# Kernel optimization log

Hardware: AMD Instinct MI355X
Metric: run time of the kernel (lower is better)

## Reference

```python
import jax, jax.numpy as jnp
import numpy as np

B, L, H, T, C = 4, 256, 768, 16, 6
SIM_THR = 0.0
EPS_LN = 1e-5


def layer_norm(x, g, b):
    m = x.mean(-1, keepdims=True)
    v = ((x - m) ** 2).mean(-1, keepdims=True)
    return (x - m) / jnp.sqrt(v + EPS_LN) * g + b


def setup_inputs() -> dict:
    key = jax.random.key(0)
    ks = jax.random.split(key, 20)
    s = 0.02
    embeddings = jax.random.normal(ks[0], (B, L, H), jnp.float32)
    masks = jnp.ones((B, L, L), jnp.float32)
    asp_st = jax.random.randint(ks[1], (B, T), 0, 12)
    asp_ed = asp_st + jax.random.randint(ks[2], (B, T), 0, 3)
    opi_st = jax.random.randint(ks[3], (B, T), 0, 12)
    opi_ed = opi_st + jax.random.randint(ks[4], (B, T), 0, 3)
    sent_id = jax.random.randint(ks[5], (B, T), 2, 5)
    return {
        "embeddings": embeddings, "masks": masks,
        "asp_st": asp_st, "asp_ed": asp_ed, "opi_st": opi_st, "opi_ed": opi_ed,
        "sent_id": sent_id,
        "edge_embed": jax.random.normal(ks[6], (2, H), jnp.float32) * s,
        "W_tp": jax.random.normal(ks[7], (2 * H + 3, H), jnp.float32) * s,
        "b_tp": jnp.zeros((H,), jnp.float32),
        "W_attn": jax.random.normal(ks[8], (3 * H, 1), jnp.float32) * s,
        "b_attn": jnp.zeros((1,), jnp.float32),
        "W_gat": jax.random.normal(ks[9], (2 * H, H), jnp.float32) * s,
        "b_gat": jnp.zeros((H,), jnp.float32),
        "gamma0": jnp.ones((H,), jnp.float32), "beta0": jnp.zeros((H,), jnp.float32),
        "W1": jax.random.normal(ks[10], (2 * H, L), jnp.float32) * s,
        "bl1": jnp.zeros((L,), jnp.float32),
        "gamma1": jnp.ones((L,), jnp.float32), "beta1": jnp.zeros((L,), jnp.float32),
        "Wc": jax.random.normal(ks[11], (L, C), jnp.float32) * s,
        "bc": jnp.zeros((C,), jnp.float32),
        "Wc1": jax.random.normal(ks[12], (L, 2), jnp.float32) * s,
        "bc1": jnp.zeros((2,), jnp.float32),
    }


def _triplet_enhance(emb_b, a_st, a_ed, o_st, o_ed, sid,
                     edge_embed, W_tp, b_tp, W_attn, b_attn, W_gat, b_gat):
    # emb_b: [L,H]; span ints: [T]
    pos = jnp.arange(L)
    am = (pos[None, :] >= a_st[:, None]) & (pos[None, :] <= a_ed[:, None])  # [T,L]
    om = (pos[None, :] >= o_st[:, None]) & (pos[None, :] <= o_ed[:, None])
    amf = am.astype(emb_b.dtype)
    omf = om.astype(emb_b.dtype)
    asp = (amf @ emb_b) / amf.sum(1, keepdims=True)  # [T,H] span-mean
    opi = (omf @ emb_b) / omf.sum(1, keepdims=True)
    sv = jax.nn.one_hot(sid - 2, 3, dtype=emb_b.dtype)  # [T,3]
    nf = jnp.concatenate([asp, opi, sv], -1) @ W_tp + b_tp  # [T,H]

    # cosine similarity between triplet nodes
    nrm = nf / jnp.maximum(jnp.linalg.norm(nf, axis=-1, keepdims=True), 1e-8)
    sim = nrm @ nrm.T
    eye = jnp.eye(T, dtype=bool)
    ok = (sim > SIM_THR) & ~eye
    m0 = ok & (a_st[:, None] == a_st[None, :]) & (a_ed[:, None] == a_ed[None, :])
    m1 = ok & (o_st[:, None] == o_st[None, :]) & (o_ed[:, None] == o_ed[None, :])
    # edge (i,j): src=i, tgt=j -> incoming mask indexed [tgt, src, etype]
    emask = jnp.stack([m0.T, m1.T], axis=-1)  # [T,T,2]

    E = edge_embed  # [2,H]
    cc = jnp.concatenate([
        jnp.broadcast_to(nf[:, None, None, :], (T, T, 2, H)),   # target feats
        jnp.broadcast_to(nf[None, :, None, :], (T, T, 2, H)),   # source feats
        jnp.broadcast_to(E[None, None, :, :], (T, T, 2, H)),
    ], -1)  # [T,T,2,3H]
    scores = (jax.nn.leaky_relu(cc, 0.2) @ W_attn)[..., 0] + b_attn[0]  # [T,T,2]
    neg = jnp.where(emask, scores, -1e9)
    attn = jax.nn.softmax(neg.reshape(T, -1), axis=-1).reshape(T, T, 2)
    msg = jnp.concatenate([
        jnp.broadcast_to(nf[:, None, :], (T, 2, H)),
        jnp.broadcast_to(E[None, :, :], (T, 2, H)),
    ], -1)  # [src, etype, 2H]
    agg = jnp.einsum('tse,sef->tf', attn, msg)
    upd = jax.nn.relu(agg @ W_gat + b_gat)
    has_in = emask.any(axis=(1, 2))
    new_nf = jnp.where(has_in[:, None], upd, nf)
    has_edges = emask.any().astype(emb_b.dtype)  # original skips scatter if no edges
    center = (a_st + o_st) // 2
    return emb_b.at[center].add(new_nf * has_edges)


def reference(embeddings, masks, asp_st, asp_ed, opi_st, opi_ed, sent_id,
              edge_embed, W_tp, b_tp, W_attn, b_attn, W_gat, b_gat,
              gamma0, beta0, W1, bl1, gamma1, beta1, Wc, bc, Wc1, bc1):
    emb1 = layer_norm(embeddings, gamma0, beta0)
    emb = jax.vmap(_triplet_enhance,
                   in_axes=(0, 0, 0, 0, 0, 0) + (None,) * 7)(
        emb1, asp_st, asp_ed, opi_st, opi_ed, sent_id,
        edge_embed, W_tp, b_tp, W_attn, b_attn, W_gat, b_gat)

    # cat([feat_exp, feat_expT]) @ W1  ==  emb@W1[:H] (rows) + emb@W1[H:] (cols)
    A = jnp.einsum('bih,hk->bik', emb, W1[:H])
    Bm = jnp.einsum('bjh,hk->bjk', emb, W1[H:])
    hidden = A[:, :, None, :] + Bm[:, None, :, :] + bl1  # [B,L,L,L]
    hidden = jax.nn.gelu(layer_norm(hidden, gamma1, beta1), approximate=False)
    logits = (hidden @ Wc + bc) * masks[..., None]    # [B,L,L,C]
    logits1 = (hidden @ Wc1 + bc1) * masks[..., None]  # [B,L,L,2]
    return jnp.concatenate([logits, logits1], -1)
```

## Files before the change

### kernel.cpp

```cpp
#include <hip/hip_runtime.h>

__device__ __forceinline__ unsigned short f2bf(float f) {
    union { float f; unsigned u; } v; v.f = f;
    unsigned u = v.u;
    unsigned r = (u + 0x7fffu + ((u >> 16) & 1u)) >> 16;
    return (unsigned short)r;
}
__device__ __forceinline__ float bfup(int x) {
    union { unsigned u; float f; } v; v.u = ((unsigned)(unsigned short)x) << 16; return v.f;
}

typedef __attribute__((ext_vector_type(8))) short short8;
typedef __attribute__((ext_vector_type(4))) float floatx4;

#define Bn 4
#define Ln 256
#define Hn 768
#define Tn 16
#define PITCH 288
#define PN 784

__global__ __launch_bounds__(256) void k_pre(const float* __restrict__ x,
                                             const float* __restrict__ g,
                                             const float* __restrict__ be,
                                             float* __restrict__ out,
                                             const float* __restrict__ W1,
                                             unsigned short* __restrict__ w1t,
                                             const float* __restrict__ Wc,
                                             const float* __restrict__ Wc1,
                                             const float* __restrict__ g1,
                                             const float* __restrict__ b1,
                                             unsigned short* __restrict__ wfg,
                                             const int* __restrict__ ast_, const int* __restrict__ aed_,
                                             const int* __restrict__ ost_, const int* __restrict__ oed_,
                                             const int* __restrict__ sid_,
                                             float* __restrict__ xv,
                                             float* __restrict__ nf,
                                             float* __restrict__ hedge) {
    int bid = blockIdx.x, tid = threadIdx.x;
    if (bid < 1024) {
        int row = bid;
        const float* xr = x + (size_t)row * Hn;
        float v0 = xr[tid], v1 = xr[tid + 256], v2 = xr[tid + 512];
        float s = v0 + v1 + v2;
        float q = v0 * v0 + v1 * v1 + v2 * v2;
        __shared__ float sm[4], qm[4];
        for (int o = 32; o > 0; o >>= 1) { s += __shfl_down(s, o); q += __shfl_down(q, o); }
        if ((tid & 63) == 0) { sm[tid >> 6] = s; qm[tid >> 6] = q; }
        __syncthreads();
        float S = sm[0] + sm[1] + sm[2] + sm[3];
        float Q = qm[0] + qm[1] + qm[2] + qm[3];
        float mean = S * (1.f / 768.f);
        float rstd = rsqrtf(Q * (1.f / 768.f) - mean * mean + 1e-5f);
        float* o0 = out + (size_t)row * Hn;
        o0[tid]       = (v0 - mean) * rstd * g[tid]       + be[tid];
        o0[tid + 256] = (v1 - mean) * rstd * g[tid + 256] + be[tid + 256];
        o0[tid + 512] = (v2 - mean) * rstd * g[tid + 512] + be[tid + 512];
    } else if (bid < 1408) {
        __shared__ float tile[32][33];
        int idx = bid - 1024;
        int kt = idx % 24, nt = idx / 24;
        int k0 = kt * 32, n0 = nt * 32;
        int rowoff = (n0 < 256) ? 0 : 768;
        int col0 = n0 & 255;
        int r = tid >> 3, c = (tid & 7) * 4;
        float4 v = *(const float4*)(W1 + (size_t)(rowoff + k0 + r) * 256 + col0 + c);
        tile[r][c] = v.x; tile[r][c + 1] = v.y; tile[r][c + 2] = v.z; tile[r][c + 3] = v.w;
        __syncthreads();
        ushort4 o;
        o.x = f2bf(tile[c][r]); o.y = f2bf(tile[c + 1][r]);
        o.z = f2bf(tile[c + 2][r]); o.w = f2bf(tile[c + 3][r]);
        *(ushort4*)(w1t + (size_t)(n0 + r) * 768 + k0 + c) = o;
    } else if (bid == 1408) {
#pragma unroll
        for (int u = 0; u < 2; ++u) {
            int e = tid + u * 256;
            int s = e >> 6, l = e & 63;
            int qq2 = l >> 4, nn2 = l & 15;
            short8 wv;
#pragma unroll
            for (int t = 0; t < 8; ++t) {
                int k = s * 32 + qq2 * 8 + t;
                float v = (nn2 < 6) ? Wc[k * 6 + nn2] : ((nn2 < 8) ? Wc1[k * 2 + (nn2 - 6)] : 0.f);
                wv[t] = (short)f2bf(v);
            }
            *(short8*)(wfg + e * 8) = wv;
        }
        wfg[4096 + tid] = f2bf(g1[tid]);
        wfg[4352 + tid] = f2bf(b1[tid]);
        if (tid < 4) hedge[tid] = 0.f;
    } else {
        __shared__ float rstdA[3], rstdO[3], cc[2];
        __shared__ float sred[4], qred[4];
        int n = bid - 1409, b = n >> 4;
        int ast = ast_[n], aed = aed_[n], ost = ost_[n], oed = oed_[n], sid = sid_[n];
        int na = aed - ast + 1, no2 = oed - ost + 1;
        if (tid == 0) { cc[0] = 0.f; cc[1] = 0.f; }
        __syncthreads();
        for (int slot = 0; slot < 6; ++slot) {
            int isA = slot < 3;
            int off = isA ? slot : slot - 3;
            int cnt = isA ? na : no2;
            int row = (isA ? ast : ost) + off;
            if (off < cnt) {
                const float* xr = x + (size_t)(b * 256 + row) * Hn;
                float v0 = xr[tid], v1 = xr[tid + 256], v2 = xr[tid + 512];
                float s = v0 + v1 + v2;
                float q = v0 * v0 + v1 * v1 + v2 * v2;
                for (int o = 32; o > 0; o >>= 1) { s += __shfl_down(s, o); q += __shfl_down(q, o); }
                if ((tid & 63) == 0) { sred[tid >> 6] = s; qred[tid >> 6] = q; }
            }
            __syncthreads();
            if (off < cnt && tid == 0) {
                float S = sred[0] + sred[1] + sred[2] + sred[3];
                float Q = qred[0] + qred[1] + qred[2] + qred[3];
                float mean = S * (1.f / 768.f);
                float rstd = rsqrtf(Q * (1.f / 768.f) - mean * mean + 1e-5f);
                if (isA) { rstdA[off] = rstd; cc[0] += mean * rstd; }
                else     { rstdO[off] = rstd; cc[1] += mean * rstd; }
            }
            __syncthreads();
        }
        float ai = 1.f / (float)na, oi = 1.f / (float)no2;
        float cA = cc[0] * ai, cO = cc[1] * oi;
        float* xrr = xv + (size_t)n * 1568;
        const float* eb = x + (size_t)b * Ln * Hn;
        for (int r = tid; r < 1568; r += 256) {
            float v;
            if (r < 768) {
                float sa = 0.f;
                for (int l = 0; l < na; ++l) sa = fmaf(eb[(ast + l) * Hn + r], rstdA[l], sa);
                v = fmaf(g[r], sa * ai - cA, be[r]);
            } else if (r < 1536) {
                int h = r - 768;
                float so = 0.f;
                for (int l = 0; l < no2; ++l) so = fmaf(eb[(ost + l) * Hn + h], rstdO[l], so);
                v = fmaf(g[h], so * oi - cO, be[h]);
            } else if (r < 1539) {
                v = (sid - 2 == r - 1536) ? 1.f : 0.f;
            } else {
                v = 0.f;
            }
            xrr[r] = v;
        }
        float* nr = nf + (size_t)n * Hn;
        nr[tid] = 0.f; nr[tid + 256] = 0.f; nr[tid + 512] = 0.f;
    }
}

__global__ __launch_bounds__(256) void k_skinny(const float* __restrict__ A,
                                                const float* __restrict__ B,
                                                const float* __restrict__ bias,
                                                float* __restrict__ C,
                                                int Kpad, int Kb, int Kc) {
    __shared__ float At[32][33], Bt[32][33];
    int tid = threadIdx.x;
    int n0 = blockIdx.x * 32, m0 = blockIdx.y * 32, z = blockIdx.z;
    int kbeg = z * Kc;
    int kend = kbeg + Kc; if (kend > Kpad) kend = Kpad;
    int lr = tid >> 3, lc = (tid & 7) * 4;
    int tm = tid >> 3, tn4 = (tid & 7) * 4;
    float acc0 = 0.f, acc1 = 0.f, acc2 = 0.f, acc3 = 0.f;
    for (int k0 = kbeg; k0 < kend; k0 += 32) {
        float4 av = *(const float4*)(A + (size_t)(m0 + lr) * Kpad + k0 + lc);
        At[lr][lc] = av.x; At[lr][lc + 1] = av.y; At[lr][lc + 2] = av.z; At[lr][lc + 3] = av.w;
        int gk = k0 + lr;
        float4 bv = {0.f, 0.f, 0.f, 0.f};
        if (gk < Kb) bv = *(const float4*)(B + (size_t)gk * 768 + n0 + lc);
        Bt[lr][lc] = bv.x; Bt[lr][lc + 1] = bv.y; Bt[lr][lc + 2] = bv.z; Bt[lr][lc + 3] = bv.w;
        __syncthreads();
#pragma unroll
        for (int k = 0; k < 32; ++k) {
            float a = At[tm][k];
            acc0 = fmaf(a, Bt[k][tn4], acc0);
            acc1 = fmaf(a, Bt[k][tn4 + 1], acc1);
            acc2 = fmaf(a, Bt[k][tn4 + 2], acc2);
            acc3 = fmaf(a, Bt[k][tn4 + 3], acc3);
        }
        __syncthreads();
    }
    if (z == 0) {
        acc0 += bias[n0 + tn4];
        acc1 += bias[n0 + tn4 + 1];
        acc2 += bias[n0 + tn4 + 2];
        acc3 += bias[n0 + tn4 + 3];
    }
    float* dst = C + (size_t)(m0 + tm) * 768 + n0 + tn4;
    atomicAdd(&dst[0], acc0);
    atomicAdd(&dst[1], acc1);
    atomicAdd(&dst[2], acc2);
    atomicAdd(&dst[3], acc3);
}

__global__ __launch_bounds__(256) void k_graph(const float* __restrict__ nf,
                                               const int* __restrict__ ast_, const int* __restrict__ aed_,
                                               const int* __restrict__ ost_, const int* __restrict__ oed_,
                                               const float* __restrict__ E,
                                               const float* __restrict__ Wat,
                                               const float* __restrict__ bat,
                                               int* __restrict__ hasin, float* __restrict__ hasedge,
                                               float* __restrict__ agg, float* __restrict__ raw) {
    int n = blockIdx.x, b = n >> 4, t = n & 15, tid = threadIdx.x;
    __shared__ float nfs[16][PN];
    __shared__ float dotS[16], n2S[16], qS[16];
    __shared__ float pT_s, rr0_s, rr1_s;
    __shared__ int asts[16], aeds[16], osts[16], oeds[16];
    __shared__ float wss[16];
    __shared__ float aes0, aes1;
    const float* nfb = nf + (size_t)b * 16 * Hn;
    if (tid < 16) {
        int m = b * 16 + tid;
        asts[tid] = ast_[m]; aeds[tid] = aed_[m];
        osts[tid] = ost_[m]; oeds[tid] = oed_[m];
    }
    int s = tid >> 4, l = tid & 15;
    const float* vs = nfb + (size_t)s * Hn;
    const float* vt = nfb + (size_t)t * Hn;
    const float* er = E + ((s == 2) ? 768 : 0);
    float d = 0.f, n2 = 0.f, qq = 0.f, pp = 0.f, rr = 0.f;
#pragma unroll 4
    for (int h = l; h < 768; h += 16) {
        float v = vs[h];
        float tv = vt[h];
        nfs[s][h] = v;
        d  = fmaf(tv, v, d);
        n2 = fmaf(v, v, n2);
        float lv = v > 0.f ? v : 0.2f * v;
        qq = fmaf(lv, Wat[768 + h], qq);
        if (s == 0) { float lt = tv > 0.f ? tv : 0.2f * tv; pp = fmaf(lt, Wat[h], pp); }
        if (s == 1 || s == 2) { float ev = er[h]; float le = ev > 0.f ? ev : 0.2f * ev; rr = fmaf(le, Wat[1536 + h], rr); }
    }
    for (int o = 8; o > 0; o >>= 1) {
        d  += __shfl_down(d, o);  n2 += __shfl_down(n2, o);
        qq += __shfl_down(qq, o); pp += __shfl_down(pp, o);
        rr += __shfl_down(rr, o);
    }
    if (l == 0) {
        dotS[s] = d; n2S[s] = n2; qS[s] = qq;
        if (s == 0) pT_s = pp;
        if (s == 1) rr0_s = rr;
        if (s == 2) rr1_s = rr;
    }
    __syncthreads();
    if (tid < 64) {
        int ss = tid >> 1, e = tid & 1;
        bool valid = tid < 32;
        int ssc = ss & 15;
        float nt = sqrtf(n2S[t]);
        float ns = sqrtf(n2S[ssc]);
        float sim = dotS[ssc] / (fmaxf(nt, 1e-8f) * fmaxf(ns, 1e-8f));
        bool ok = valid && (sim > 0.f) && (ssc != t);
        bool edge;
        if (e == 0) edge = ok && (asts[t] == asts[ssc]) && (aeds[t] == aeds[ssc]);
        else        edge = ok && (osts[t] == osts[ssc]) && (oeds[t] == oeds[ssc]);
        float sc = edge ? (pT_s + qS[ssc] + (e ? rr1_s : rr0_s) + bat[0]) : -1e9f;
        float mx = sc;
        for (int o = 16; o > 0; o >>= 1) mx = fmaxf(mx, __shfl_xor(mx, o));
        float ex = __expf(sc - mx);
        float sum = ex;
        for (int o = 16; o > 0; o >>= 1) sum += __shfl_xor(sum, o);
        float w = ex / sum;
        float wtot = w + __shfl_xor(w, 1);
        if (valid && e == 0) wss[ss] = wtot;
        float a0 = (valid && e == 0) ? w : 0.f;
        float a1 = (valid && e == 1) ? w : 0.f;
        for (int o = 16; o > 0; o >>= 1) { a0 += __shfl_xor(a0, o); a1 += __shfl_xor(a1, o); }
        unsigned long long bal = __ballot(edge);
        if (tid == 0) {
            aes0 = a0; aes1 = a1;
            int hi = (bal != 0ull) ? 1 : 0;
            hasin[n] = hi;
            if (hi) atomicAdd(&hasedge[b], 1.f);
        }
    }
    __syncthreads();
    float ae0 = aes0, ae1 = aes1;
    float* ag = agg + (size_t)n * 1536;
    float* rw = raw + (size_t)n * Hn;
    for (int f = tid; f < 768; f += 256) {
        float acc = 0.f;
#pragma unroll
        for (int s16 = 0; s16 < 16; ++s16) acc = fmaf(wss[s16], nfs[s16][f], acc);
        ag[f] = acc;
        ag[768 + f] = ae0 * E[f] + ae1 * E[768 + f];
        rw[f] = 0.f;
    }
}

__global__ __launch_bounds__(256) void k_scatter(const float* __restrict__ raw,
                                                 const float* __restrict__ nf,
                                                 const int* __restrict__ hasin, const float* __restrict__ hasedge,
                                                 const int* __restrict__ ast_, const int* __restrict__ ost_,
                                                 float* __restrict__ emb) {
    int n = blockIdx.x, b = n >> 4, tid = threadIdx.x;
    if (hasedge[b] == 0.f) return;
    int center = (ast_[n] + ost_[n]) >> 1;
    float* dst = emb + (size_t)(b * Ln + center) * Hn;
    int hi = hasin[n];
    const float* src = hi ? (raw + (size_t)n * Hn) : (nf + (size_t)n * Hn);
    for (int h = tid; h < 768; h += 256) {
        float v = src[h];
        if (hi) v = fmaxf(v, 0.f);
        atomicAdd(&dst[h], v);
    }
}

__global__ __launch_bounds__(64) void k_gemm(const float* __restrict__ emb,
                                             const unsigned short* __restrict__ w1t,
                                             float* __restrict__ abm) {
    int wid = blockIdx.x;
    int m0 = (wid >> 4) * 32;
    int n0 = (wid & 15) * 32;
    int lane = threadIdx.x;
    int r = lane & 15, g = lane >> 4;
    const float* Af0 = emb + (size_t)(m0 + r) * 768 + g * 8;
    const float* Af1 = emb + (size_t)(m0 + 16 + r) * 768 + g * 8;
    const short8* Bp0 = (const short8*)(w1t + (size_t)(n0 + r) * 768 + g * 8);
    const short8* Bp1 = (const short8*)(w1t + (size_t)(n0 + 16 + r) * 768 + g * 8);
    floatx4 acc00 = {0.f, 0.f, 0.f, 0.f}, acc01 = {0.f, 0.f, 0.f, 0.f};
    floatx4 acc10 = {0.f, 0.f, 0.f, 0.f}, acc11 = {0.f, 0.f, 0.f, 0.f};
#pragma unroll 4
    for (int ks = 0; ks < 768; ks += 32) {
        float4 x0 = *(const float4*)(Af0 + ks);
        float4 x1 = *(const float4*)(Af0 + ks + 4);
        float4 y0 = *(const float4*)(Af1 + ks);
        float4 y1 = *(const float4*)(Af1 + ks + 4);
        short8 a0, a1;
        union { float f; unsigned u; } cv;
#define PK(dst, idx, val) { cv.f = (val); dst[idx] = (short)((cv.u + 0x8000u) >> 16); }
        PK(a0, 0, x0.x) PK(a0, 1, x0.y) PK(a0, 2, x0.z) PK(a0, 3, x0.w)
        PK(a0, 4, x1.x) PK(a0, 5, x1.y) PK(a0, 6, x1.z) PK(a0, 7, x1.w)
        PK(a1, 0, y0.x) PK(a1, 1, y0.y) PK(a1, 2, y0.z) PK(a1, 3, y0.w)
        PK(a1, 4, y1.x) PK(a1, 5, y1.y) PK(a1, 6, y1.z) PK(a1, 7, y1.w)
#undef PK
        short8 b0 = Bp0[ks >> 3];
        short8 b1 = Bp1[ks >> 3];
        acc00 = __builtin_amdgcn_mfma_f32_16x16x32_bf16(a0, b0, acc00, 0, 0, 0);
        acc01 = __builtin_amdgcn_mfma_f32_16x16x32_bf16(a0, b1, acc01, 0, 0, 0);
        acc10 = __builtin_amdgcn_mfma_f32_16x16x32_bf16(a1, b0, acc10, 0, 0, 0);
        acc11 = __builtin_amdgcn_mfma_f32_16x16x32_bf16(a1, b1, acc11, 0, 0, 0);
    }
#pragma unroll
    for (int t = 0; t < 4; ++t) {
        int row = g * 4 + t;
        abm[(size_t)(m0 + row) * 512 + n0 + r]           = acc00[t];
        abm[(size_t)(m0 + row) * 512 + n0 + 16 + r]      = acc01[t];
        abm[(size_t)(m0 + 16 + row) * 512 + n0 + r]      = acc10[t];
        abm[(size_t)(m0 + 16 + row) * 512 + n0 + 16 + r] = acc11[t];
    }
}

__global__ __launch_bounds__(256) void k_hidden3(const float* __restrict__ abm,
                                                 const float* __restrict__ bl1,
                                                 const float* __restrict__ masks,
                                                 const unsigned short* __restrict__ wfg,
                                                 const float* __restrict__ bc,
                                                 const float* __restrict__ bc1,
                                                 float* __restrict__ out) {
    __shared__ unsigned short As[16][PITCH];
    __shared__ unsigned short Bs[16][PITCH];
    __shared__ unsigned short gsh[256], bsh[256];
    __shared__ short8 Wf[8][64];
    __shared__ float Ds[16][16];
    __shared__ float ms[16][16];
    __shared__ float sAs[16], qAs[16], sBs[16], qBs[16];
    int tid = threadIdx.x;
    int jt = blockIdx.x, it = blockIdx.y, b = blockIdx.z;
    int rowA = b * 256 + it * 16;
    int rowB = b * 256 + jt * 16;
    {
        int r = tid >> 4, sg = tid & 15;
        const float* Ar = abm + (size_t)(rowA + r) * 512 + sg * 16;
        const float* Br = abm + (size_t)(rowB + r) * 512 + 256 + sg * 16;
        const float* Lr = bl1 + sg * 16;
        float sa = 0.f, qa = 0.f, sb = 0.f, qb = 0.f;
        short8 va0, va1, vb0, vb1;
#pragma unroll
        for (int u = 0; u < 4; ++u) {
            float4 av = *(const float4*)(Ar + u * 4);
            float4 bv = *(const float4*)(Br + u * 4);
            float4 lv = *(const float4*)(Lr + u * 4);
            float aa[4] = {av.x, av.y, av.z, av.w};
            float bb[4] = {bv.x + lv.x, bv.y + lv.y, bv.z + lv.z, bv.w + lv.w};
#pragma unroll
            for (int e = 0; e < 4; ++e) {
                unsigned short ah = f2bf(aa[e]), bh = f2bf(bb[e]);
                float af = bfup(ah), bf2 = bfup(bh);
                sa += af; qa = fmaf(af, af, qa);
                sb += bf2; qb = fmaf(bf2, bf2, qb);
                int pos = u * 4 + e;
                if (pos < 8) { va0[pos] = (short)ah; vb0[pos] = (short)bh; }
                else         { va1[pos - 8] = (short)ah; vb1[pos - 8] = (short)bh; }
            }
        }
        *(short8*)&As[r][sg * 16]     = va0;
        *(short8*)&As[r][sg * 16 + 8] = va1;
        *(short8*)&Bs[r][sg * 16]     = vb0;
        *(short8*)&Bs[r][sg * 16 + 8] = vb1;
        for (int o = 8; o > 0; o >>= 1) {
            sa += __shfl_down(sa, o); qa += __shfl_down(qa, o);
            sb += __shfl_down(sb, o); qb += __shfl_down(qb, o);
        }
        if (sg == 0) { sAs[r] = sa; qAs[r] = qa; sBs[r] = sb; qBs[r] = qb; }
    }
#pragma unroll
    for (int u = 0; u < 2; ++u) {
        int e = tid + u * 256;
        ((short8*)Wf)[e] = *(const short8*)(wfg + e * 8);
    }
    gsh[tid] = wfg[4096 + tid];
    bsh[tid] = wfg[4352 + tid];
    {
        int di = tid >> 4, dj = tid & 15;
        ms[di][dj] = masks[((size_t)(b * 256 + it * 16 + di)) * 256 + jt * 16 + dj];
    }
    __syncthreads();
    if (tid < 64) {
        int m = tid & 15, q = tid >> 4;
        floatx4 acc = {0.f, 0.f, 0.f, 0.f};
#pragma unroll
        for (int s = 0; s < 8; ++s) {
            short8 a8 = *(const short8*)&As[m][s * 32 + q * 8];
            short8 b8 = *(const short8*)&Bs[m][s * 32 + q * 8];
            acc = __builtin_amdgcn_mfma_f32_16x16x32_bf16(a8, b8, acc, 0, 0, 0);
        }
#pragma unroll
        for (int rg = 0; rg < 4; ++rg) Ds[q * 4 + rg][m] = acc[rg];
    }
    __syncthreads();

    int lane = tid & 63, w = tid >> 6;
    int m = lane & 15, q = lane >> 4;
    int iA = w * 4 + (m & 3);
    int jB0 = m >> 2;
    int n = m;
    float bcs_l = (n < 6) ? bc[n] : ((n < 8) ? bc1[n - 6] : 0.f);
    const float inv256 = 1.f / 256.f;
    const float K1 = -1.5957691216f, K2 = -0.0713548163f;

    float rr4[4], cc4[4];
#pragma unroll
    for (int p = 0; p < 4; ++p) {
        int jB = p * 4 + jB0;
        float mu = (sAs[iA] + sBs[jB]) * inv256;
        float E2 = (qAs[iA] + 2.f * Ds[iA][jB] + qBs[jB]) * inv256;
        float r_ = rsqrtf(E2 - mu * mu + 1e-5f);
        rr4[p] = r_;
        cc4[p] = -mu * r_;
    }
    floatx4 acc0 = {0.f, 0.f, 0.f, 0.f};
    floatx4 acc1 = {0.f, 0.f, 0.f, 0.f};
    floatx4 acc2 = {0.f, 0.f, 0.f, 0.f};
    floatx4 acc3 = {0.f, 0.f, 0.f, 0.f};

#pragma unroll 2
    for (int s = 0; s < 8; ++s) {
        int ko = s * 32 + q * 8;
        short8 a8 = *(const short8*)&As[iA][ko];
        short8 g8 = *(const short8*)&gsh[ko];
        short8 v8 = *(const short8*)&bsh[ko];
        short8 wv = Wf[s][lane];
        float af[8], gf[8], vf[8];
#pragma unroll
        for (int t = 0; t < 8; ++t) { af[t] = bfup(a8[t]); gf[t] = bfup(g8[t]); vf[t] = bfup(v8[t]); }
#define PSTEP(P, ACC) do {                                                        \
        short8 b8 = *(const short8*)&Bs[P * 4 + jB0][ko];                         \
        float r_ = rr4[P], c_ = cc4[P];                                           \
        short8 yv;                                                                \
        _Pragma("unroll")                                                         \
        for (int t = 0; t < 8; ++t) {                                             \
            float x = fmaf(af[t] + bfup(b8[t]), r_, c_);                          \
            x = fmaf(x, gf[t], vf[t]);                                            \
            float mm = fmaf(x * x, K2, K1);                                       \
            float e = __expf(x * mm);                                             \
            float y = x * __builtin_amdgcn_rcpf(1.f + e);                         \
            union { float f; unsigned u; } cv; cv.f = y;                          \
            yv[t] = (short)((cv.u + 0x8000u) >> 16);                              \
        }                                                                         \
        ACC = __builtin_amdgcn_mfma_f32_16x16x32_bf16(yv, wv, ACC, 0, 0, 0);      \
    } while (0)
        PSTEP(0, acc0);
        PSTEP(1, acc1);
        PSTEP(2, acc2);
        PSTEP(3, acc3);
#undef PSTEP
    }

    if (n < 8) {
#pragma unroll
        for (int rg = 0; rg < 4; ++rg) {
            int mp = q * 4 + rg;
            int il = w * 4 + (mp & 3);
            int base_j = mp >> 2;
            size_t rowbase = ((size_t)(b * 256 + it * 16 + il)) * 256 + jt * 16;
            {
                int jl = 0 * 4 + base_j;
                out[(rowbase + jl) * 8 + n] = (acc0[rg] + bcs_l) * ms[il][jl];
            }
            {
                int jl = 1 * 4 + base_j;
                out[(rowbase + jl) * 8 + n] = (acc1[rg] + bcs_l) * ms[il][jl];
            }
            {
                int jl = 2 * 4 + base_j;
                out[(rowbase + jl) * 8 + n] = (acc2[rg] + bcs_l) * ms[il][jl];
            }
            {
                int jl = 3 * 4 + base_j;
                out[(rowbase + jl) * 8 + n] = (acc3[rg] + bcs_l) * ms[il][jl];
            }
        }
    }
}

extern "C" void kernel_launch(void* const* d_in, const int* in_sizes, int n_in,
                              void* d_out, int out_size, void* d_ws, size_t ws_size,
                              hipStream_t stream) {
    (void)in_sizes; (void)n_in; (void)out_size; (void)ws_size;
    const float* emb_in = (const float*)d_in[0];
    const float* masks  = (const float*)d_in[1];
    const int* ast = (const int*)d_in[2];
    const int* aed = (const int*)d_in[3];
    const int* ost = (const int*)d_in[4];
    const int* oed = (const int*)d_in[5];
    const int* sid = (const int*)d_in[6];
    const float* E    = (const float*)d_in[7];
    const float* Wtp  = (const float*)d_in[8];
    const float* btp  = (const float*)d_in[9];
    const float* Wat  = (const float*)d_in[10];
    const float* bat  = (const float*)d_in[11];
    const float* Wg   = (const float*)d_in[12];
    const float* bg   = (const float*)d_in[13];
    const float* g0   = (const float*)d_in[14];
    const float* b0   = (const float*)d_in[15];
    const float* W1   = (const float*)d_in[16];
    const float* bl1  = (const float*)d_in[17];
    const float* g1   = (const float*)d_in[18];
    const float* b1   = (const float*)d_in[19];
    const float* Wc   = (const float*)d_in[20];
    const float* bc   = (const float*)d_in[21];
    const float* Wc1  = (const float*)d_in[22];
    const float* bc1  = (const float*)d_in[23];
    float* outp = (float*)d_out;

    float* fw = (float*)d_ws;
    float* emb = fw;
    float* nf  = fw + 786432;
    int*   hasin = (int*)(fw + 835584);
    float* hasedge = fw + 835648;
    float* xv  = fw + 835712;
    float* agg = fw + 936064;
    float* raw = fw + 1034368;
    float* abm = fw + 1083520;
    unsigned short* w1t = (unsigned short*)(fw + 1607808);
    unsigned short* wfg = (unsigned short*)(fw + 1804416);

    k_pre<<<1473, 256, 0, stream>>>(emb_in, g0, b0, emb, W1, w1t,
                                    Wc, Wc1, g1, b1, wfg,
                                    ast, aed, ost, oed, sid, xv, nf, hasedge);
    dim3 gs1(24, 2, 7);
    k_skinny<<<gs1, 256, 0, stream>>>(xv, Wtp, btp, nf, 1568, 1539, 224);
    k_graph<<<64, 256, 0, stream>>>(nf, ast, aed, ost, oed, E, Wat, bat, hasin, hasedge, agg, raw);
    k_skinny<<<gs1, 256, 0, stream>>>(agg, Wg, bg, raw, 1536, 1536, 224);
    k_scatter<<<64, 256, 0, stream>>>(raw, nf, hasin, hasedge, ast, ost, emb);
    k_gemm<<<512, 64, 0, stream>>>(emb, w1t, abm);
    dim3 g6(16, 16, 4);
    k_hidden3<<<g6, 256, 0, stream>>>(abm, bl1, masks, wfg, bc, bc1, outp);
}
```

Measured before the change: 225.7 us.

## Fuse six pre-GEMM kernels into one persistent kernel with grid barriers

Replaces the six launches k_pre, k_skinny, k_graph, k_skinny, k_scatter and k_gemm with a single persistent kernel of 256 blocks. The phases are separated by atomic-counter grid barriers, and the counters are zeroed by a memset before launch. The aim is to remove per-launch overhead and inter-kernel gaps on small phases. The cost is reduced parallelism in the first phase (1473 work items looped over 256 blocks), spin-wait barriers that rely on all blocks being co-resident, and an extra memset call.

```diff
diff --git a/kernel.cpp b/kernel.cpp
--- a/kernel.cpp
+++ b/kernel.cpp
@@ -19,154 +19,64 @@
 #define Tn 16
 #define PITCH 288
 #define PN 784
-
-__global__ __launch_bounds__(256) void k_pre(const float* __restrict__ x,
-                                             const float* __restrict__ g,
-                                             const float* __restrict__ be,
-                                             float* __restrict__ out,
-                                             const float* __restrict__ W1,
-                                             unsigned short* __restrict__ w1t,
-                                             const float* __restrict__ Wc,
-                                             const float* __restrict__ Wc1,
-                                             const float* __restrict__ g1,
-                                             const float* __restrict__ b1,
-                                             unsigned short* __restrict__ wfg,
-                                             const int* __restrict__ ast_, const int* __restrict__ aed_,
-                                             const int* __restrict__ ost_, const int* __restrict__ oed_,
-                                             const int* __restrict__ sid_,
-                                             float* __restrict__ xv,
-                                             float* __restrict__ nf,
-                                             float* __restrict__ hedge) {
-    int bid = blockIdx.x, tid = threadIdx.x;
-    if (bid < 1024) {
-        int row = bid;
-        const float* xr = x + (size_t)row * Hn;
-        float v0 = xr[tid], v1 = xr[tid + 256], v2 = xr[tid + 512];
-        float s = v0 + v1 + v2;
-        float q = v0 * v0 + v1 * v1 + v2 * v2;
-        __shared__ float sm[4], qm[4];
-        for (int o = 32; o > 0; o >>= 1) { s += __shfl_down(s, o); q += __shfl_down(q, o); }
-        if ((tid & 63) == 0) { sm[tid >> 6] = s; qm[tid >> 6] = q; }
-        __syncthreads();
-        float S = sm[0] + sm[1] + sm[2] + sm[3];
-        float Q = qm[0] + qm[1] + qm[2] + qm[3];
-        float mean = S * (1.f / 768.f);
-        float rstd = rsqrtf(Q * (1.f / 768.f) - mean * mean + 1e-5f);
-        float* o0 = out + (size_t)row * Hn;
-        o0[tid]       = (v0 - mean) * rstd * g[tid]       + be[tid];
-        o0[tid + 256] = (v1 - mean) * rstd * g[tid + 256] + be[tid + 256];
-        o0[tid + 512] = (v2 - mean) * rstd * g[tid + 512] + be[tid + 512];
-    } else if (bid < 1408) {
-        __shared__ float tile[32][33];
-        int idx = bid - 1024;
-        int kt = idx % 24, nt = idx / 24;
-        int k0 = kt * 32, n0 = nt * 32;
-        int rowoff = (n0 < 256) ? 0 : 768;
-        int col0 = n0 & 255;
-        int r = tid >> 3, c = (tid & 7) * 4;
-        float4 v = *(const float4*)(W1 + (size_t)(rowoff + k0 + r) * 256 + col0 + c);
-        tile[r][c] = v.x; tile[r][c + 1] = v.y; tile[r][c + 2] = v.z; tile[r][c + 3] = v.w;
-        __syncthreads();
-        ushort4 o;
-        o.x = f2bf(tile[c][r]); o.y = f2bf(tile[c + 1][r]);
-        o.z = f2bf(tile[c + 2][r]); o.w = f2bf(tile[c + 3][r]);
-        *(ushort4*)(w1t + (size_t)(n0 + r) * 768 + k0 + c) = o;
-    } else if (bid == 1408) {
-#pragma unroll
-        for (int u = 0; u < 2; ++u) {
-            int e = tid + u * 256;
-            int s = e >> 6, l = e & 63;
-            int qq2 = l >> 4, nn2 = l & 15;
-            short8 wv;
-#pragma unroll
-            for (int t = 0; t < 8; ++t) {
-                int k = s * 32 + qq2 * 8 + t;
-                float v = (nn2 < 6) ? Wc[k * 6 + nn2] : ((nn2 < 8) ? Wc1[k * 2 + (nn2 - 6)] : 0.f);
-                wv[t] = (short)f2bf(v);
-            }
-            *(short8*)(wfg + e * 8) = wv;
-        }
-        wfg[4096 + tid] = f2bf(g1[tid]);
-        wfg[4352 + tid] = f2bf(b1[tid]);
-        if (tid < 4) hedge[tid] = 0.f;
-    } else {
-        __shared__ float rstdA[3], rstdO[3], cc[2];
-        __shared__ float sred[4], qred[4];
-        int n = bid - 1409, b = n >> 4;
-        int ast = ast_[n], aed = aed_[n], ost = ost_[n], oed = oed_[n], sid = sid_[n];
-        int na = aed - ast + 1, no2 = oed - ost + 1;
-        if (tid == 0) { cc[0] = 0.f; cc[1] = 0.f; }
-        __syncthreads();
-        for (int slot = 0; slot < 6; ++slot) {
-            int isA = slot < 3;
-            int off = isA ? slot : slot - 3;
-            int cnt = isA ? na : no2;
-            int row = (isA ? ast : ost) + off;
-            if (off < cnt) {
-                const float* xr = x + (size_t)(b * 256 + row) * Hn;
-                float v0 = xr[tid], v1 = xr[tid + 256], v2 = xr[tid + 512];
-                float s = v0 + v1 + v2;
-                float q = v0 * v0 + v1 * v1 + v2 * v2;
-                for (int o = 32; o > 0; o >>= 1) { s += __shfl_down(s, o); q += __shfl_down(q, o); }
-                if ((tid & 63) == 0) { sred[tid >> 6] = s; qred[tid >> 6] = q; }
-            }
-            __syncthreads();
-            if (off < cnt && tid == 0) {
-                float S = sred[0] + sred[1] + sred[2] + sred[3];
-                float Q = qred[0] + qred[1] + qred[2] + qred[3];
-                float mean = S * (1.f / 768.f);
-                float rstd = rsqrtf(Q * (1.f / 768.f) - mean * mean + 1e-5f);
-                if (isA) { rstdA[off] = rstd; cc[0] += mean * rstd; }
-                else     { rstdO[off] = rstd; cc[1] += mean * rstd; }
-            }
-            __syncthreads();
-        }
-        float ai = 1.f / (float)na, oi = 1.f / (float)no2;
-        float cA = cc[0] * ai, cO = cc[1] * oi;
-        float* xrr = xv + (size_t)n * 1568;
-        const float* eb = x + (size_t)b * Ln * Hn;
-        for (int r = tid; r < 1568; r += 256) {
-            float v;
-            if (r < 768) {
-                float sa = 0.f;
-                for (int l = 0; l < na; ++l) sa = fmaf(eb[(ast + l) * Hn + r], rstdA[l], sa);
-                v = fmaf(g[r], sa * ai - cA, be[r]);
-            } else if (r < 1536) {
-                int h = r - 768;
-                float so = 0.f;
-                for (int l = 0; l < no2; ++l) so = fmaf(eb[(ost + l) * Hn + h], rstdO[l], so);
-                v = fmaf(g[h], so * oi - cO, be[h]);
-            } else if (r < 1539) {
-                v = (sid - 2 == r - 1536) ? 1.f : 0.f;
-            } else {
-                v = 0.f;
-            }
-            xrr[r] = v;
-        }
-        float* nr = nf + (size_t)n * Hn;
-        nr[tid] = 0.f; nr[tid + 256] = 0.f; nr[tid + 512] = 0.f;
-    }
-}
-
-__global__ __launch_bounds__(256) void k_skinny(const float* __restrict__ A,
-                                                const float* __restrict__ B,
-                                                const float* __restrict__ bias,
-                                                float* __restrict__ C,
-                                                int Kpad, int Kb, int Kc) {
-    __shared__ float At[32][33], Bt[32][33];
-    int tid = threadIdx.x;
-    int n0 = blockIdx.x * 32, m0 = blockIdx.y * 32, z = blockIdx.z;
+#define NBLK 256
+
+struct MidArgs {
+    const float* x;
+    const float* g0; const float* b0;
+    float* emb;
+    const float* W1; unsigned short* w1t;
+    const float* Wc; const float* Wc1; const float* g1; const float* b1;
+    unsigned short* wfg;
+    const int* ast; const int* aed; const int* ost; const int* oed; const int* sid;
+    float* xv; float* nf; float* hedge;
+    const float* Wtp; const float* btp;
+    const float* E; const float* Wat; const float* bat;
+    int* hasin; float* agg; float* raw;
+    const float* Wg; const float* bg;
+    float* abm;
+    unsigned* bar;
+};
+
+#define SMEM_F 12704
+
+__device__ __forceinline__ void gbar(unsigned* cnt, int tid) {
+    __syncthreads();
+    if (tid == 0) {
+        __threadfence();
+        __hip_atomic_fetch_add(cnt, 1u, __ATOMIC_ACQ_REL, __HIP_MEMORY_SCOPE_AGENT);
+        unsigned spins = 0;
+        while (__hip_atomic_load(cnt, __ATOMIC_ACQUIRE, __HIP_MEMORY_SCOPE_AGENT) < NBLK) {
+            __builtin_amdgcn_s_sleep(2);
+            if (++spins > 400000000u) break;
+        }
+    }
+    __syncthreads();
+}
+
+
+__device__ __forceinline__ void skinny_tile(const float* __restrict__ Ain,
+                                            const float* __restrict__ Bin,
+                                            const float* __restrict__ bias,
+                                            float* __restrict__ C,
+                                            int Kpad, int Kb, int Kc,
+                                            int blk, int tid, float* sh) {
+    float (*At)[33] = (float(*)[33])sh;
+    float (*Bt)[33] = (float(*)[33])(sh + 1056);
+    int n0 = (blk % 24) * 32;
+    int m0 = ((blk / 24) & 1) * 32;
+    int z = blk / 48;
     int kbeg = z * Kc;
     int kend = kbeg + Kc; if (kend > Kpad) kend = Kpad;
     int lr = tid >> 3, lc = (tid & 7) * 4;
     int tm = tid >> 3, tn4 = (tid & 7) * 4;
     float acc0 = 0.f, acc1 = 0.f, acc2 = 0.f, acc3 = 0.f;
     for (int k0 = kbeg; k0 < kend; k0 += 32) {
-        float4 av = *(const float4*)(A + (size_t)(m0 + lr) * Kpad + k0 + lc);
+        float4 av = *(const float4*)(Ain + (size_t)(m0 + lr) * Kpad + k0 + lc);
         At[lr][lc] = av.x; At[lr][lc + 1] = av.y; At[lr][lc + 2] = av.z; At[lr][lc + 3] = av.w;
         int gk = k0 + lr;
         float4 bv = {0.f, 0.f, 0.f, 0.f};
-        if (gk < Kb) bv = *(const float4*)(B + (size_t)gk * 768 + n0 + lc);
+        if (gk < Kb) bv = *(const float4*)(Bin + (size_t)gk * 768 + n0 + lc);
         Bt[lr][lc] = bv.x; Bt[lr][lc + 1] = bv.y; Bt[lr][lc + 2] = bv.z; Bt[lr][lc + 3] = bv.w;
         __syncthreads();
 #pragma unroll
@@ -192,31 +102,29 @@
     atomicAdd(&dst[3], acc3);
 }
 
-__global__ __launch_bounds__(256) void k_graph(const float* __restrict__ nf,
-                                               const int* __restrict__ ast_, const int* __restrict__ aed_,
-                                               const int* __restrict__ ost_, const int* __restrict__ oed_,
-                                               const float* __restrict__ E,
-                                               const float* __restrict__ Wat,
-                                               const float* __restrict__ bat,
-                                               int* __restrict__ hasin, float* __restrict__ hasedge,
-                                               float* __restrict__ agg, float* __restrict__ raw) {
-    int n = blockIdx.x, b = n >> 4, t = n & 15, tid = threadIdx.x;
-    __shared__ float nfs[16][PN];
-    __shared__ float dotS[16], n2S[16], qS[16];
-    __shared__ float pT_s, rr0_s, rr1_s;
-    __shared__ int asts[16], aeds[16], osts[16], oeds[16];
-    __shared__ float wss[16];
-    __shared__ float aes0, aes1;
-    const float* nfb = nf + (size_t)b * 16 * Hn;
+__device__ __forceinline__ void graph_body(const MidArgs& A, int blk, int tid, float* sh) {
+    int n = blk, b = n >> 4, t = n & 15;
+    float (*nfs)[PN] = (float(*)[PN])sh;
+    float* dotS = sh + 12544;
+    float* n2S  = dotS + 16;
+    float* qS   = n2S + 16;
+    float* misc = qS + 16;
+    float* wss  = misc + 3;
+    float* aes  = wss + 16;
+    int* asts = (int*)(aes + 2);
+    int* aeds = asts + 16;
+    int* osts = aeds + 16;
+    int* oeds = osts + 16;
+    const float* nfb = A.nf + (size_t)b * 16 * Hn;
     if (tid < 16) {
         int m = b * 16 + tid;
-        asts[tid] = ast_[m]; aeds[tid] = aed_[m];
-        osts[tid] = ost_[m]; oeds[tid] = oed_[m];
+        asts[tid] = A.ast[m]; aeds[tid] = A.aed[m];
+        osts[tid] = A.ost[m]; oeds[tid] = A.oed[m];
     }
     int s = tid >> 4, l = tid & 15;
     const float* vs = nfb + (size_t)s * Hn;
     const float* vt = nfb + (size_t)t * Hn;
-    const float* er = E + ((s == 2) ? 768 : 0);
+    const float* er = A.E + ((s == 2) ? 768 : 0);
     float d = 0.f, n2 = 0.f, qq = 0.f, pp = 0.f, rr = 0.f;
 #pragma unroll 4
     for (int h = l; h < 768; h += 16) {
@@ -226,9 +134,9 @@
         d  = fmaf(tv, v, d);
         n2 = fmaf(v, v, n2);
         float lv = v > 0.f ? v : 0.2f * v;
-        qq = fmaf(lv, Wat[768 + h], qq);
-        if (s == 0) { float lt = tv > 0.f ? tv : 0.2f * tv; pp = fmaf(lt, Wat[h], pp); }
-        if (s == 1 || s == 2) { float ev = er[h]; float le = ev > 0.f ? ev : 0.2f * ev; rr = fmaf(le, Wat[1536 + h], rr); }
+        qq = fmaf(lv, A.Wat[768 + h], qq);
+        if (s == 0) { float lt = tv > 0.f ? tv : 0.2f * tv; pp = fmaf(lt, A.Wat[h], pp); }
+        if (s == 1 || s == 2) { float ev = er[h]; float le = ev > 0.f ? ev : 0.2f * ev; rr = fmaf(le, A.Wat[1536 + h], rr); }
     }
     for (int o = 8; o > 0; o >>= 1) {
         d  += __shfl_down(d, o);  n2 += __shfl_down(n2, o);
@@ -237,9 +145,9 @@
     }
     if (l == 0) {
         dotS[s] = d; n2S[s] = n2; qS[s] = qq;
-        if (s == 0) pT_s = pp;
-        if (s == 1) rr0_s = rr;
-        if (s == 2) rr1_s = rr;
+        if (s == 0) misc[0] = pp;
+        if (s == 1) misc[1] = rr;
+        if (s == 2) misc[2] = rr;
     }
     __syncthreads();
     if (tid < 64) {
@@ -253,7 +161,7 @@
         bool edge;
         if (e == 0) edge = ok && (asts[t] == asts[ssc]) && (aeds[t] == aeds[ssc]);
         else        edge = ok && (osts[t] == osts[ssc]) && (oeds[t] == oeds[ssc]);
-        float sc = edge ? (pT_s + qS[ssc] + (e ? rr1_s : rr0_s) + bat[0]) : -1e9f;
+        float sc = edge ? (misc[0] + qS[ssc] + (e ? misc[2] : misc[1]) + A.bat[0]) : -1e9f;
         float mx = sc;
         for (int o = 16; o > 0; o >>= 1) mx = fmaxf(mx, __shfl_xor(mx, o));
         float ex = __expf(sc - mx);
@@ -267,51 +175,30 @@
         for (int o = 16; o > 0; o >>= 1) { a0 += __shfl_xor(a0, o); a1 += __shfl_xor(a1, o); }
         unsigned long long bal = __ballot(edge);
         if (tid == 0) {
-            aes0 = a0; aes1 = a1;
+            aes[0] = a0; aes[1] = a1;
             int hi = (bal != 0ull) ? 1 : 0;
-            hasin[n] = hi;
-            if (hi) atomicAdd(&hasedge[b], 1.f);
+            A.hasin[n] = hi;
+            if (hi) atomicAdd(&A.hedge[b], 1.f);
         }
     }
     __syncthreads();
-    float ae0 = aes0, ae1 = aes1;
-    float* ag = agg + (size_t)n * 1536;
-    float* rw = raw + (size_t)n * Hn;
+    float ae0 = aes[0], ae1 = aes[1];
+    float* ag = A.agg + (size_t)n * 1536;
     for (int f = tid; f < 768; f += 256) {
         float acc = 0.f;
 #pragma unroll
         for (int s16 = 0; s16 < 16; ++s16) acc = fmaf(wss[s16], nfs[s16][f], acc);
         ag[f] = acc;
-        ag[768 + f] = ae0 * E[f] + ae1 * E[768 + f];
-        rw[f] = 0.f;
-    }
-}
-
-__global__ __launch_bounds__(256) void k_scatter(const float* __restrict__ raw,
-                                                 const float* __restrict__ nf,
-                                                 const int* __restrict__ hasin, const float* __restrict__ hasedge,
-                                                 const int* __restrict__ ast_, const int* __restrict__ ost_,
-                                                 float* __restrict__ emb) {
-    int n = blockIdx.x, b = n >> 4, tid = threadIdx.x;
-    if (hasedge[b] == 0.f) return;
-    int center = (ast_[n] + ost_[n]) >> 1;
-    float* dst = emb + (size_t)(b * Ln + center) * Hn;
-    int hi = hasin[n];
-    const float* src = hi ? (raw + (size_t)n * Hn) : (nf + (size_t)n * Hn);
-    for (int h = tid; h < 768; h += 256) {
-        float v = src[h];
-        if (hi) v = fmaxf(v, 0.f);
-        atomicAdd(&dst[h], v);
-    }
-}
-
-__global__ __launch_bounds__(64) void k_gemm(const float* __restrict__ emb,
-                                             const unsigned short* __restrict__ w1t,
-                                             float* __restrict__ abm) {
-    int wid = blockIdx.x;
+        ag[768 + f] = ae0 * A.E[f] + ae1 * A.E[768 + f];
+    }
+}
+
+__device__ __forceinline__ void gemm_wave(const float* __restrict__ emb,
+                                          const unsigned short* __restrict__ w1t,
+                                          float* __restrict__ abm,
+                                          int wid, int lane) {
     int m0 = (wid >> 4) * 32;
     int n0 = (wid & 15) * 32;
-    int lane = threadIdx.x;
     int r = lane & 15, g = lane >> 4;
     const float* Af0 = emb + (size_t)(m0 + r) * 768 + g * 8;
     const float* Af1 = emb + (size_t)(m0 + 16 + r) * 768 + g * 8;
@@ -348,6 +235,158 @@
         abm[(size_t)(m0 + 16 + row) * 512 + n0 + r]      = acc10[t];
         abm[(size_t)(m0 + 16 + row) * 512 + n0 + 16 + r] = acc11[t];
     }
+}
+
+__global__ __launch_bounds__(256) void k_mid(MidArgs A) {
+    __shared__ float sh[SMEM_F];
+    int blk = blockIdx.x, tid = threadIdx.x;
+
+    for (int j = blk; j < 1473; j += NBLK) {
+        __syncthreads();
+        if (j < 1024) {
+            int row = j;
+            const float* xr = A.x + (size_t)row * Hn;
+            float v0 = xr[tid], v1 = xr[tid + 256], v2 = xr[tid + 512];
+            float s = v0 + v1 + v2;
+            float q = v0 * v0 + v1 * v1 + v2 * v2;
+            float* sm = sh; float* qm = sh + 4;
+            for (int o = 32; o > 0; o >>= 1) { s += __shfl_down(s, o); q += __shfl_down(q, o); }
+            if ((tid & 63) == 0) { sm[tid >> 6] = s; qm[tid >> 6] = q; }
+            __syncthreads();
+            float S = sm[0] + sm[1] + sm[2] + sm[3];
+            float Q = qm[0] + qm[1] + qm[2] + qm[3];
+            float mean = S * (1.f / 768.f);
+            float rstd = rsqrtf(Q * (1.f / 768.f) - mean * mean + 1e-5f);
+            float* o0 = A.emb + (size_t)row * Hn;
+            o0[tid]       = (v0 - mean) * rstd * A.g0[tid]       + A.b0[tid];
+            o0[tid + 256] = (v1 - mean) * rstd * A.g0[tid + 256] + A.b0[tid + 256];
+            o0[tid + 512] = (v2 - mean) * rstd * A.g0[tid + 512] + A.b0[tid + 512];
+        } else if (j < 1408) {
+            float (*tile)[33] = (float(*)[33])sh;
+            int idx = j - 1024;
+            int kt = idx % 24, nt = idx / 24;
+            int k0 = kt * 32, n0 = nt * 32;
+            int rowoff = (n0 < 256) ? 0 : 768;
+            int col0 = n0 & 255;
+            int r = tid >> 3, c = (tid & 7) * 4;
+            float4 v = *(const float4*)(A.W1 + (size_t)(rowoff + k0 + r) * 256 + col0 + c);
+            tile[r][c] = v.x; tile[r][c + 1] = v.y; tile[r][c + 2] = v.z; tile[r][c + 3] = v.w;
+            __syncthreads();
+            ushort4 o;
+            o.x = f2bf(tile[c][r]); o.y = f2bf(tile[c + 1][r]);
+            o.z = f2bf(tile[c + 2][r]); o.w = f2bf(tile[c + 3][r]);
+            *(ushort4*)(A.w1t + (size_t)(n0 + r) * 768 + k0 + c) = o;
+        } else if (j == 1408) {
+#pragma unroll
+            for (int u = 0; u < 2; ++u) {
+                int e = tid + u * 256;
+                int s = e >> 6, l = e & 63;
+                int qq2 = l >> 4, nn2 = l & 15;
+                short8 wv;
+#pragma unroll
+                for (int t = 0; t < 8; ++t) {
+                    int k = s * 32 + qq2 * 8 + t;
+                    float v = (nn2 < 6) ? A.Wc[k * 6 + nn2] : ((nn2 < 8) ? A.Wc1[k * 2 + (nn2 - 6)] : 0.f);
+                    wv[t] = (short)f2bf(v);
+                }
+                *(short8*)(A.wfg + e * 8) = wv;
+            }
+            A.wfg[4096 + tid] = f2bf(A.g1[tid]);
+            A.wfg[4352 + tid] = f2bf(A.b1[tid]);
+            if (tid < 4) A.hedge[tid] = 0.f;
+        } else {
+            float* rstdA = sh;
+            float* rstdO = sh + 3;
+            float* cc    = sh + 6;
+            float* sred  = sh + 8;
+            float* qred  = sh + 12;
+            int n = j - 1409, b = n >> 4;
+            int a_st = A.ast[n], a_ed = A.aed[n], o_st = A.ost[n], o_ed = A.oed[n], s_id = A.sid[n];
+            int na = a_ed - a_st + 1, no2 = o_ed - o_st + 1;
+            if (tid == 0) { cc[0] = 0.f; cc[1] = 0.f; }
+            __syncthreads();
+            for (int slot = 0; slot < 6; ++slot) {
+                int isA = slot < 3;
+                int off = isA ? slot : slot - 3;
+                int cnt = isA ? na : no2;
+                int row = (isA ? a_st : o_st) + off;
+                if (off < cnt) {
+                    const float* xr = A.x + (size_t)(b * 256 + row) * Hn;
+                    float v0 = xr[tid], v1 = xr[tid + 256], v2 = xr[tid + 512];
+                    float s = v0 + v1 + v2;
+                    float q = v0 * v0 + v1 * v1 + v2 * v2;
+                    for (int o = 32; o > 0; o >>= 1) { s += __shfl_down(s, o); q += __shfl_down(q, o); }
+                    if ((tid & 63) == 0) { sred[tid >> 6] = s; qred[tid >> 6] = q; }
+                }
+                __syncthreads();
+                if (off < cnt && tid == 0) {
+                    float S = sred[0] + sred[1] + sred[2] + sred[3];
+                    float Q = qred[0] + qred[1] + qred[2] + qred[3];
+                    float mean = S * (1.f / 768.f);
+                    float rstd = rsqrtf(Q * (1.f / 768.f) - mean * mean + 1e-5f);
+                    if (isA) { rstdA[off] = rstd; cc[0] += mean * rstd; }
+                    else     { rstdO[off] = rstd; cc[1] += mean * rstd; }
+                }
+                __syncthreads();
+            }
+            float ai = 1.f / (float)na, oi = 1.f / (float)no2;
+            float cA = cc[0] * ai, cO = cc[1] * oi;
+            float* xrr = A.xv + (size_t)n * 1568;
+            const float* eb = A.x + (size_t)b * Ln * Hn;
+            for (int r = tid; r < 1568; r += 256) {
+                float v;
+                if (r < 768) {
+                    float sa = 0.f;
+                    for (int l = 0; l < na; ++l) sa = fmaf(eb[(a_st + l) * Hn + r], rstdA[l], sa);
+                    v = fmaf(A.g0[r], sa * ai - cA, A.b0[r]);
+                } else if (r < 1536) {
+                    int h = r - 768;
+                    float so = 0.f;
+                    for (int l = 0; l < no2; ++l) so = fmaf(eb[(o_st + l) * Hn + h], rstdO[l], so);
+                    v = fmaf(A.g0[h], so * oi - cO, A.b0[h]);
+                } else if (r < 1539) {
+                    v = (s_id - 2 == r - 1536) ? 1.f : 0.f;
+                } else {
+                    v = 0.f;
+                }
+                xrr[r] = v;
+            }
+            float* nr = A.nf + (size_t)n * Hn;
+            nr[tid] = 0.f; nr[tid + 256] = 0.f; nr[tid + 512] = 0.f;
+            float* rw2 = A.raw + (size_t)n * Hn;
+            rw2[tid] = 0.f; rw2[tid + 256] = 0.f; rw2[tid + 512] = 0.f;
+        }
+    }
+    gbar(A.bar + 0, tid);
+
+    for (int j = blk; j < 336; j += NBLK)
+        skinny_tile(A.xv, A.Wtp, A.btp, A.nf, 1568, 1539, 224, j, tid, sh);
+    gbar(A.bar + 1, tid);
+
+    if (blk < 64) graph_body(A, blk, tid, sh);
+    gbar(A.bar + 2, tid);
+
+    for (int j = blk; j < 336; j += NBLK)
+        skinny_tile(A.agg, A.Wg, A.bg, A.raw, 1536, 1536, 224, j, tid, sh);
+    gbar(A.bar + 3, tid);
+
+    if (blk < 64) {
+        int n = blk, b = n >> 4;
+        if (A.hedge[b] != 0.f) {
+            int center = (A.ast[n] + A.ost[n]) >> 1;
+            float* dst = A.emb + (size_t)(b * Ln + center) * Hn;
+            int hi = A.hasin[n];
+            const float* src = hi ? (A.raw + (size_t)n * Hn) : (A.nf + (size_t)n * Hn);
+            for (int h = tid; h < 768; h += 256) {
+                float v = src[h];
+                if (hi) v = fmaxf(v, 0.f);
+                atomicAdd(&dst[h], v);
+            }
+        }
+    }
+    gbar(A.bar + 4, tid);
+
+    if (blk < 128) gemm_wave(A.emb, A.w1t, A.abm, blk * 4 + (tid >> 6), tid & 63);
 }
 
 __global__ __launch_bounds__(256) void k_hidden3(const float* __restrict__ abm,
@@ -554,16 +593,27 @@
     float* abm = fw + 1083520;
     unsigned short* w1t = (unsigned short*)(fw + 1607808);
     unsigned short* wfg = (unsigned short*)(fw + 1804416);
-
-    k_pre<<<1473, 256, 0, stream>>>(emb_in, g0, b0, emb, W1, w1t,
-                                    Wc, Wc1, g1, b1, wfg,
-                                    ast, aed, ost, oed, sid, xv, nf, hasedge);
-    dim3 gs1(24, 2, 7);
-    k_skinny<<<gs1, 256, 0, stream>>>(xv, Wtp, btp, nf, 1568, 1539, 224);
-    k_graph<<<64, 256, 0, stream>>>(nf, ast, aed, ost, oed, E, Wat, bat, hasin, hasedge, agg, raw);
-    k_skinny<<<gs1, 256, 0, stream>>>(agg, Wg, bg, raw, 1536, 1536, 224);
-    k_scatter<<<64, 256, 0, stream>>>(raw, nf, hasin, hasedge, ast, ost, emb);
-    k_gemm<<<512, 64, 0, stream>>>(emb, w1t, abm);
+    unsigned* bar = (unsigned*)(fw + 1806720);
+
+    hipMemsetAsync((void*)bar, 0, 64, stream);
+
+    MidArgs ma;
+    ma.x = emb_in; ma.g0 = g0; ma.b0 = b0;
+    ma.emb = emb;
+    ma.W1 = W1; ma.w1t = w1t;
+    ma.Wc = Wc; ma.Wc1 = Wc1; ma.g1 = g1; ma.b1 = b1;
+    ma.wfg = wfg;
+    ma.ast = ast; ma.aed = aed; ma.ost = ost; ma.oed = oed; ma.sid = sid;
+    ma.xv = xv; ma.nf = nf; ma.hedge = hasedge;
+    ma.Wtp = Wtp; ma.btp = btp;
+    ma.E = E; ma.Wat = Wat; ma.bat = bat;
+    ma.hasin = hasin; ma.agg = agg; ma.raw = raw;
+    ma.Wg = Wg; ma.bg = bg;
+    ma.abm = abm;
+    ma.bar = bar;
+
+    k_mid<<<NBLK, 256, 0, stream>>>(ma);
+
     dim3 g6(16, 16, 4);
     k_hidden3<<<g6, 256, 0, stream>>>(abm, bl1, masks, wfg, bc, bc1, outp);
 }
```

New measurement: 462.3 us. +104.9%, slower.
